# Kernel optimization log

Measured on AMD Instinct MI355X. Metric: run time of the kernel, lower is better.

## Reference

```python
import jax, jax.numpy as jnp
import numpy as np
import math

S, B, L, D = 4096, 2048, 256, 128  # substructure pool, batch, max substructs/drug, hidden


def setup_inputs() -> dict:
    key = jax.random.key(0)
    ks = jax.random.split(key, 6)
    sub_feat = jax.random.normal(ks[0], (S, D), dtype=jnp.float32)
    sub_index = jax.random.randint(ks[1], (B, L), 0, S)
    # ragged lengths -> padded prefix mask (1.0 = valid substructure)
    lengths = jax.random.randint(ks[2], (B,), 8, L + 1)
    mask = (jnp.arange(L)[None, :] < lengths[:, None]).astype(jnp.float32)
    scale = 1.0 / math.sqrt(D)
    Wq = jax.random.normal(ks[3], (D, D), dtype=jnp.float32) * scale
    Wk = jax.random.normal(ks[4], (D, D), dtype=jnp.float32) * scale
    bq = jnp.zeros((D,), dtype=jnp.float32)
    bk = jnp.zeros((D,), dtype=jnp.float32)
    return {"sub_feat": sub_feat, "mask": mask, "Wq": Wq, "bq": bq,
            "Wk": Wk, "bk": bk, "sub_index": sub_index}


def reference(sub_feat, mask, Wq, bq, Wk, bk, sub_index):
    # per-drug gather of substructure ('expert') features: [B, L, D]
    gathered = sub_feat[sub_index]
    # single-head Q/K projections (V is computed but unused in the original)
    q = gathered @ Wq + bq  # [B, L, D]
    k = gathered @ Wk + bk  # [B, L, D]
    inv_sqrt_d = 1.0 / math.sqrt(D)
    # additive mask: (1 - m) * -10000 broadcast over query dim
    add_mask = (1.0 - mask)[:, None, :] * -10000.0  # [B, 1, L]
    scores = jnp.einsum('bid,bjd->bij', q, k) * inv_sqrt_d + add_mask  # [B, L, L]
    probs = jax.nn.softmax(scores, axis=-1)
    # O[:, 0, 0, :] in the original: head 0, query position 0
    score = probs[:, 0, :]  # [B, L]
    # drug_feat[i] = score[i] @ sub_feat[sub_index[i]]
    drug_embeddings = jnp.einsum('bl,bld->bd', score, gathered)  # [B, D]
    return drug_embeddings
```

## Files before the change

kernel.cpp:

```cpp
#include <hip/hip_runtime.h>

#define DIM 128
#define LEN 256
#define INV_SQRT_D 0.08838834764831845f
#define LOG2E 1.4426950408889634f
#define SCALE_L2 (INV_SQRT_D * LOG2E)

#define WS_MT   0
#define WS_C    (DIM * DIM)
#define WS_W2   (DIM * DIM + DIM)
#define WS_BQBK (DIM * DIM + 2 * DIM)
#define WS_VBUF (DIM * DIM + 2 * DIM + 8)

__global__ __launch_bounds__(128) void precompute_kernel(
    const float* __restrict__ Wq, const float* __restrict__ bq,
    const float* __restrict__ Wk, const float* __restrict__ bk,
    float* __restrict__ ws)
{
    const int t = threadIdx.x;
    const int j = blockIdx.x;
    if (j < DIM) {
        __shared__ float wqj[DIM];
        wqj[t] = Wq[j * DIM + t];
        __syncthreads();
        const float4* row = reinterpret_cast<const float4*>(Wk + t * DIM);
        float acc = 0.f;
        #pragma unroll 8
        for (int i = 0; i < DIM / 4; ++i) {
            float4 u = row[i];
            acc = fmaf(u.x, wqj[4*i+0], acc);
            acc = fmaf(u.y, wqj[4*i+1], acc);
            acc = fmaf(u.z, wqj[4*i+2], acc);
            acc = fmaf(u.w, wqj[4*i+3], acc);
        }
        ws[WS_MT + j * DIM + t] = acc;
    } else {
        __shared__ float bqs[DIM], bks[DIM], red[DIM];
        bqs[t] = bq[t]; bks[t] = bk[t];
        __syncthreads();
        const float4* rk = reinterpret_cast<const float4*>(Wk + t * DIM);
        const float4* rq = reinterpret_cast<const float4*>(Wq + t * DIM);
        float accC = 0.f, accW = 0.f;
        #pragma unroll 8
        for (int i = 0; i < DIM / 4; ++i) {
            float4 a  = rk[i];
            float4 b2 = rq[i];
            accC = fmaf(a.x,  bqs[4*i+0], accC);
            accC = fmaf(a.y,  bqs[4*i+1], accC);
            accC = fmaf(a.z,  bqs[4*i+2], accC);
            accC = fmaf(a.w,  bqs[4*i+3], accC);
            accW = fmaf(b2.x, bks[4*i+0], accW);
            accW = fmaf(b2.y, bks[4*i+1], accW);
            accW = fmaf(b2.z, bks[4*i+2], accW);
            accW = fmaf(b2.w, bks[4*i+3], accW);
        }
        ws[WS_C  + t] = accC;
        ws[WS_W2 + t] = accW;
        red[t] = bqs[t] * bks[t];
        __syncthreads();
        if (t == 0) {
            float s = 0.f;
            for (int i = 0; i < DIM; ++i) s += red[i];
            ws[WS_BQBK] = s;
        }
    }
}

__global__ __launch_bounds__(256) void vcompute_kernel(
    const float* __restrict__ sub_feat, const int* __restrict__ sub_index,
    const float* __restrict__ ws, float* __restrict__ vout,
    float* __restrict__ qout, int B)
{
    const int t    = threadIdx.x;
    const int lane = t & 63;
    const int wv   = t >> 6;

    __shared__ float MtL[DIM * DIM];
    __shared__ float g0L[4][DIM];

    const float4* Msrc = reinterpret_cast<const float4*>(ws + WS_MT);
    float4* Mdst = reinterpret_cast<float4*>(MtL);
    #pragma unroll
    for (int i = 0; i < 16; ++i) Mdst[t + 256 * i] = Msrc[t + 256 * i];
    __syncthreads();

    const float* w2 = ws + WS_W2;
    const float* cc = ws + WS_C;
    const float  bqbk = ws[WS_BQBK];

    #pragma unroll
    for (int s = 0; s < 2; ++s) {
        const int b = blockIdx.x * 8 + wv * 2 + s;
        if (b >= B) break;
        const int r0 = sub_index[(size_t)b * LEN];
        const float2 g0p = reinterpret_cast<const float2*>(sub_feat + (size_t)r0 * DIM)[lane];
        g0L[wv][2 * lane]     = g0p.x;
        g0L[wv][2 * lane + 1] = g0p.y;

        float qp = g0p.x * w2[2 * lane] + g0p.y * w2[2 * lane + 1];
        #pragma unroll
        for (int o = 32; o > 0; o >>= 1) qp += __shfl_xor(qp, o);
        if (lane == 0) qout[b] = qp + bqbk;

        float a0 = 0.f, a1 = 0.f;
        #pragma unroll 8
        for (int j = 0; j < DIM; ++j) {
            const float g = g0L[wv][j];
            a0 = fmaf(g, MtL[j * DIM + lane],      a0);
            a1 = fmaf(g, MtL[j * DIM + lane + 64], a1);
        }
        vout[(size_t)b * DIM + lane]      = a0 + cc[lane];
        vout[(size_t)b * DIM + lane + 64] = a1 + cc[lane + 64];
    }
}

__global__ __launch_bounds__(256) void attn_kernel(
    const float* __restrict__ sub_feat, const float* __restrict__ mask,
    const int* __restrict__ sub_index, const float* __restrict__ vbuf,
    const float* __restrict__ qbuf, float* __restrict__ out, int B)
{
    const int t    = threadIdx.x;
    const int lane = t & 63;
    const int wv   = t >> 6;
    const int pair = wv >> 1;
    const int rhalf= wv & 1;
    const int b    = blockIdx.x * 2 + pair;
    const int g    = lane >> 4;
    const int m16  = lane & 15;

    __shared__ int   idxs[4][DIM];
    __shared__ float bias[4][DIM];
    __shared__ float OW  [4][DIM];
    __shared__ float Zw  [4];

    float Zr = 0.f;
    float O0=0.f,O1=0.f,O2=0.f,O3=0.f,O4=0.f,O5=0.f,O6=0.f,O7=0.f;

    if (b < B) {
        int*   idw = idxs[wv];
        float* bw  = bias[wv];
        const int*   ib = sub_index + (size_t)b * LEN + rhalf * DIM;
        const float* mb = mask      + (size_t)b * LEN + rhalf * DIM;
        idw[lane]      = ib[lane];
        idw[lane + 64] = ib[lane + 64];
        bw[lane]       = (1.f - mb[lane])      * (-10000.f * LOG2E);
        bw[lane + 64]  = (1.f - mb[lane + 64]) * (-10000.f * LOG2E);

        const float4 vA = reinterpret_cast<const float4*>(vbuf + (size_t)b * DIM)[m16];
        const float4 vB = reinterpret_cast<const float4*>(vbuf + (size_t)b * DIM)[m16 + 16];
        const float qterm = qbuf[b] * SCALE_L2;

        #pragma unroll 4
        for (int k = 0; k < 32; ++k) {
            const int jl = 4 * k + g;
            const int ij = idw[jl];
            const float bj = bw[jl];
            const float* rp = sub_feat + (size_t)ij * DIM + 4 * m16;
            const float4 u0 = *reinterpret_cast<const float4*>(rp);
            const float4 u1 = *reinterpret_cast<const float4*>(rp + 64);
            float sd = u0.x*vA.x + u0.y*vA.y + u0.z*vA.z + u0.w*vA.w
                     + u1.x*vB.x + u1.y*vB.y + u1.z*vB.z + u1.w*vB.w;
            sd += __shfl_xor(sd, 1);
            sd += __shfl_xor(sd, 2);
            sd += __shfl_xor(sd, 4);
            sd += __shfl_xor(sd, 8);
            const float e = exp2f(sd * SCALE_L2 + qterm + bj);
            Zr += e;
            O0 = fmaf(e, u0.x, O0); O1 = fmaf(e, u0.y, O1);
            O2 = fmaf(e, u0.z, O2); O3 = fmaf(e, u0.w, O3);
            O4 = fmaf(e, u1.x, O4); O5 = fmaf(e, u1.y, O5);
            O6 = fmaf(e, u1.z, O6); O7 = fmaf(e, u1.w, O7);
        }

        #pragma unroll
        for (int msk = 16; msk <= 32; msk <<= 1) {
            Zr += __shfl_xor(Zr, msk);
            O0 += __shfl_xor(O0, msk); O1 += __shfl_xor(O1, msk);
            O2 += __shfl_xor(O2, msk); O3 += __shfl_xor(O3, msk);
            O4 += __shfl_xor(O4, msk); O5 += __shfl_xor(O5, msk);
            O6 += __shfl_xor(O6, msk); O7 += __shfl_xor(O7, msk);
        }
        if (lane < 16) {
            reinterpret_cast<float4*>(&OW[wv][0])[m16]  = make_float4(O0, O1, O2, O3);
            reinterpret_cast<float4*>(&OW[wv][64])[m16] = make_float4(O4, O5, O6, O7);
        }
        if (lane == 0) Zw[wv] = Zr;
    }
    __syncthreads();

    {
        const int p = t >> 7;
        const int d = t & (DIM - 1);
        const int ob = blockIdx.x * 2 + p;
        if (ob < B) {
            const float Zt = Zw[2*p] + Zw[2*p+1];
            out[(size_t)ob * DIM + d] = (OW[2*p][d] + OW[2*p+1][d]) / Zt;
        }
    }
}

__global__ __launch_bounds__(256) void fused_fallback(
    const float* __restrict__ sub_feat, const float* __restrict__ mask,
    const int* __restrict__ sub_index, const float* __restrict__ ws,
    float* __restrict__ out)
{
    const int t    = threadIdx.x;
    const int lane = t & 63;
    const int wv   = t >> 6;
    const int pair = wv >> 1;
    const int rhalf= wv & 1;
    const int b    = blockIdx.x * 2 + pair;
    const int c32  = lane & 31;
    const int h    = lane >> 5;
    const int g    = lane >> 4;
    const int m16  = lane & 15;

    const float* Mt = ws + WS_MT;
    const float* cc = ws + WS_C;
    const float* w2 = ws + WS_W2;

    __shared__ float g0s [4][DIM];
    __shared__ int   idxs[4][DIM];
    __shared__ float bias[4][DIM];
    __shared__ float OW  [4][DIM];
    __shared__ float Zw  [4];

    float* g0w = g0s[wv];
    int*   idw = idxs[wv];
    float* bw  = bias[wv];

    const int*   ib = sub_index + (size_t)b * LEN + rhalf * DIM;
    const float* mb = mask      + (size_t)b * LEN + rhalf * DIM;
    idw[lane]      = ib[lane];
    idw[lane + 64] = ib[lane + 64];
    bw[lane]       = (1.f - mb[lane])      * (-10000.f * LOG2E);
    bw[lane + 64]  = (1.f - mb[lane + 64]) * (-10000.f * LOG2E);

    const int r0 = sub_index[(size_t)b * LEN];
    const float2 g0p = reinterpret_cast<const float2*>(sub_feat + (size_t)r0 * DIM)[lane];
    g0w[2 * lane]     = g0p.x;
    g0w[2 * lane + 1] = g0p.y;

    float qp = g0p.x * w2[2 * lane] + g0p.y * w2[2 * lane + 1];
    #pragma unroll
    for (int o = 32; o > 0; o >>= 1) qp += __shfl_xor(qp, o);
    const float qterm = (qp + ws[WS_BQBK]) * SCALE_L2;

    float4 vacc = make_float4(0.f, 0.f, 0.f, 0.f);
    {
        const int jb = h * 64;
        #pragma unroll 8
        for (int k = 0; k < 64; ++k) {
            const int j = jb + k;
            const float gg = g0w[j];
            const float4 u = reinterpret_cast<const float4*>(Mt + j * DIM)[c32];
            vacc.x = fmaf(gg, u.x, vacc.x);
            vacc.y = fmaf(gg, u.y, vacc.y);
            vacc.z = fmaf(gg, u.z, vacc.z);
            vacc.w = fmaf(gg, u.w, vacc.w);
        }
    }
    vacc.x += __shfl_xor(vacc.x, 32);
    vacc.y += __shfl_xor(vacc.y, 32);
    vacc.z += __shfl_xor(vacc.z, 32);
    vacc.w += __shfl_xor(vacc.w, 32);
    const float4 cv = reinterpret_cast<const float4*>(cc)[c32];
    float4 vt;
    vt.x = vacc.x + cv.x; vt.y = vacc.y + cv.y;
    vt.z = vacc.z + cv.z; vt.w = vacc.w + cv.w;

    float4 vA, vB;
    vA.x = __shfl(vt.x, m16);      vA.y = __shfl(vt.y, m16);
    vA.z = __shfl(vt.z, m16);      vA.w = __shfl(vt.w, m16);
    vB.x = __shfl(vt.x, m16 + 16); vB.y = __shfl(vt.y, m16 + 16);
    vB.z = __shfl(vt.z, m16 + 16); vB.w = __shfl(vt.w, m16 + 16);

    float Zr = 0.f;
    float O0=0.f,O1=0.f,O2=0.f,O3=0.f,O4=0.f,O5=0.f,O6=0.f,O7=0.f;
    #pragma unroll 4
    for (int k = 0; k < 32; ++k) {
        const int jl = 4 * k + g;
        const int ij = idw[jl];
        const float bj = bw[jl];
        const float* rp = sub_feat + (size_t)ij * DIM + 4 * m16;
        const float4 u0 = *reinterpret_cast<const float4*>(rp);
        const float4 u1 = *reinterpret_cast<const float4*>(rp + 64);
        float sd = u0.x*vA.x + u0.y*vA.y + u0.z*vA.z + u0.w*vA.w
                 + u1.x*vB.x + u1.y*vB.y + u1.z*vB.z + u1.w*vB.w;
        sd += __shfl_xor(sd, 1);
        sd += __shfl_xor(sd, 2);
        sd += __shfl_xor(sd, 4);
        sd += __shfl_xor(sd, 8);
        const float e = exp2f(sd * SCALE_L2 + qterm + bj);
        Zr += e;
        O0 = fmaf(e, u0.x, O0); O1 = fmaf(e, u0.y, O1);
        O2 = fmaf(e, u0.z, O2); O3 = fmaf(e, u0.w, O3);
        O4 = fmaf(e, u1.x, O4); O5 = fmaf(e, u1.y, O5);
        O6 = fmaf(e, u1.z, O6); O7 = fmaf(e, u1.w, O7);
    }
    #pragma unroll
    for (int msk = 16; msk <= 32; msk <<= 1) {
        Zr += __shfl_xor(Zr, msk);
        O0 += __shfl_xor(O0, msk); O1 += __shfl_xor(O1, msk);
        O2 += __shfl_xor(O2, msk); O3 += __shfl_xor(O3, msk);
        O4 += __shfl_xor(O4, msk); O5 += __shfl_xor(O5, msk);
        O6 += __shfl_xor(O6, msk); O7 += __shfl_xor(O7, msk);
    }
    if (lane < 16) {
        reinterpret_cast<float4*>(&OW[wv][0])[m16]  = make_float4(O0, O1, O2, O3);
        reinterpret_cast<float4*>(&OW[wv][64])[m16] = make_float4(O4, O5, O6, O7);
    }
    if (lane == 0) Zw[wv] = Zr;
    __syncthreads();

    {
        const int p = t >> 7;
        const int d = t & (DIM - 1);
        const float Zt = Zw[2*p] + Zw[2*p+1];
        out[((size_t)blockIdx.x * 2 + p) * DIM + d] = (OW[2*p][d] + OW[2*p+1][d]) / Zt;
    }
}

extern "C" void kernel_launch(void* const* d_in, const int* in_sizes, int n_in,
                              void* d_out, int out_size, void* d_ws, size_t ws_size,
                              hipStream_t stream) {
    const float* sub_feat  = (const float*)d_in[0];
    const float* mask      = (const float*)d_in[1];
    const float* Wq        = (const float*)d_in[2];
    const float* bq        = (const float*)d_in[3];
    const float* Wk        = (const float*)d_in[4];
    const float* bk        = (const float*)d_in[5];
    const int*   sub_index = (const int*)d_in[6];
    float* outp = (float*)d_out;
    float* ws   = (float*)d_ws;

    const int B = in_sizes[6] / LEN;
    const size_t needed = ((size_t)WS_VBUF + (size_t)B * DIM + (size_t)B) * sizeof(float);

    precompute_kernel<<<dim3(DIM + 1), dim3(DIM), 0, stream>>>(Wq, bq, Wk, bk, ws);

    if (ws_size >= needed) {
        float* vbuf = ws + WS_VBUF;
        float* qbuf = vbuf + (size_t)B * DIM;
        vcompute_kernel<<<dim3((B + 7) / 8), dim3(256), 0, stream>>>(
            sub_feat, sub_index, ws, vbuf, qbuf, B);
        attn_kernel<<<dim3((B + 1) / 2), dim3(256), 0, stream>>>(
            sub_feat, mask, sub_index, vbuf, qbuf, outp, B);
    } else {
        fused_fallback<<<dim3(B / 2), dim3(256), 0, stream>>>(
            sub_feat, mask, sub_index, ws, outp);
    }
}
```

Before: 32.47 us.

## Gather bf16 copy of substructure features in attention and fold scale into V/q

A new kernel converts sub_feat to bf16 each call. The attention kernel then gathers 16-byte rows of 8 bf16 values instead of two float4 loads, which halves gather traffic. The softmax scale is pre-multiplied into vbuf and qbuf, which removes a multiply from the inner loop. The attention kernel is also regrouped to one drug per 256-thread block, with four waves splitting the 256 positions, and sets occupancy launch bounds. The costs are an extra launch and reduced precision of the features used in the scores and the weighted sum.

```diff
diff --git a/kernel.cpp b/kernel.cpp
--- a/kernel.cpp
+++ b/kernel.cpp
@@ -11,6 +11,9 @@
 #define WS_W2   (DIM * DIM + DIM)
 #define WS_BQBK (DIM * DIM + 2 * DIM)
 #define WS_VBUF (DIM * DIM + 2 * DIM + 8)
+
+__device__ __forceinline__ float bl(unsigned u) { return __uint_as_float(u << 16); }
+__device__ __forceinline__ float bh(unsigned u) { return __uint_as_float(u & 0xffff0000u); }
 
 __global__ __launch_bounds__(128) void precompute_kernel(
     const float* __restrict__ Wq, const float* __restrict__ bq,
@@ -66,6 +69,22 @@
     }
 }
 
+__global__ __launch_bounds__(256) void convert_kernel(
+    const float* __restrict__ src, ushort* __restrict__ dst, int n4)
+{
+    const int i = blockIdx.x * 256 + threadIdx.x;
+    if (i < n4) {
+        const float4 u = reinterpret_cast<const float4*>(src)[i];
+        ushort4 o;
+        unsigned a;
+        a = __float_as_uint(u.x); o.x = (ushort)((a + 0x7fffu + ((a >> 16) & 1u)) >> 16);
+        a = __float_as_uint(u.y); o.y = (ushort)((a + 0x7fffu + ((a >> 16) & 1u)) >> 16);
+        a = __float_as_uint(u.z); o.z = (ushort)((a + 0x7fffu + ((a >> 16) & 1u)) >> 16);
+        a = __float_as_uint(u.w); o.w = (ushort)((a + 0x7fffu + ((a >> 16) & 1u)) >> 16);
+        reinterpret_cast<ushort4*>(dst)[i] = o;
+    }
+}
+
 __global__ __launch_bounds__(256) void vcompute_kernel(
     const float* __restrict__ sub_feat, const int* __restrict__ sub_index,
     const float* __restrict__ ws, float* __restrict__ vout,
@@ -100,7 +119,7 @@
         float qp = g0p.x * w2[2 * lane] + g0p.y * w2[2 * lane + 1];
         #pragma unroll
         for (int o = 32; o > 0; o >>= 1) qp += __shfl_xor(qp, o);
-        if (lane == 0) qout[b] = qp + bqbk;
+        if (lane == 0) qout[b] = (qp + bqbk) * SCALE_L2;
 
         float a0 = 0.f, a1 = 0.f;
         #pragma unroll 8
@@ -109,93 +128,80 @@
             a0 = fmaf(g, MtL[j * DIM + lane],      a0);
             a1 = fmaf(g, MtL[j * DIM + lane + 64], a1);
         }
-        vout[(size_t)b * DIM + lane]      = a0 + cc[lane];
-        vout[(size_t)b * DIM + lane + 64] = a1 + cc[lane + 64];
-    }
-}
-
-__global__ __launch_bounds__(256) void attn_kernel(
-    const float* __restrict__ sub_feat, const float* __restrict__ mask,
+        vout[(size_t)b * DIM + lane]      = (a0 + cc[lane])      * SCALE_L2;
+        vout[(size_t)b * DIM + lane + 64] = (a1 + cc[lane + 64]) * SCALE_L2;
+    }
+}
+
+__global__ __launch_bounds__(256, 8) void attn_kernel(
+    const ushort* __restrict__ gfeat, const float* __restrict__ mask,
     const int* __restrict__ sub_index, const float* __restrict__ vbuf,
-    const float* __restrict__ qbuf, float* __restrict__ out, int B)
+    const float* __restrict__ qbuf, float* __restrict__ out)
 {
     const int t    = threadIdx.x;
     const int lane = t & 63;
     const int wv   = t >> 6;
-    const int pair = wv >> 1;
-    const int rhalf= wv & 1;
-    const int b    = blockIdx.x * 2 + pair;
+    const int b    = blockIdx.x;
     const int g    = lane >> 4;
     const int m16  = lane & 15;
 
-    __shared__ int   idxs[4][DIM];
-    __shared__ float bias[4][DIM];
-    __shared__ float OW  [4][DIM];
-    __shared__ float Zw  [4];
+    __shared__ int   idw[LEN];
+    __shared__ float bw [LEN];
+    __shared__ float OW [4][DIM];
+    __shared__ float Zw [4];
+
+    idw[t] = sub_index[(size_t)b * LEN + t];
+    bw[t]  = (1.f - mask[(size_t)b * LEN + t]) * (-10000.f * LOG2E);
+
+    const float4 va = reinterpret_cast<const float4*>(vbuf + (size_t)b * DIM)[2 * m16];
+    const float4 vb = reinterpret_cast<const float4*>(vbuf + (size_t)b * DIM)[2 * m16 + 1];
+    const float qterm = qbuf[b];
 
     float Zr = 0.f;
     float O0=0.f,O1=0.f,O2=0.f,O3=0.f,O4=0.f,O5=0.f,O6=0.f,O7=0.f;
 
-    if (b < B) {
-        int*   idw = idxs[wv];
-        float* bw  = bias[wv];
-        const int*   ib = sub_index + (size_t)b * LEN + rhalf * DIM;
-        const float* mb = mask      + (size_t)b * LEN + rhalf * DIM;
-        idw[lane]      = ib[lane];
-        idw[lane + 64] = ib[lane + 64];
-        bw[lane]       = (1.f - mb[lane])      * (-10000.f * LOG2E);
-        bw[lane + 64]  = (1.f - mb[lane + 64]) * (-10000.f * LOG2E);
-
-        const float4 vA = reinterpret_cast<const float4*>(vbuf + (size_t)b * DIM)[m16];
-        const float4 vB = reinterpret_cast<const float4*>(vbuf + (size_t)b * DIM)[m16 + 16];
-        const float qterm = qbuf[b] * SCALE_L2;
-
-        #pragma unroll 4
-        for (int k = 0; k < 32; ++k) {
-            const int jl = 4 * k + g;
-            const int ij = idw[jl];
-            const float bj = bw[jl];
-            const float* rp = sub_feat + (size_t)ij * DIM + 4 * m16;
-            const float4 u0 = *reinterpret_cast<const float4*>(rp);
-            const float4 u1 = *reinterpret_cast<const float4*>(rp + 64);
-            float sd = u0.x*vA.x + u0.y*vA.y + u0.z*vA.z + u0.w*vA.w
-                     + u1.x*vB.x + u1.y*vB.y + u1.z*vB.z + u1.w*vB.w;
-            sd += __shfl_xor(sd, 1);
-            sd += __shfl_xor(sd, 2);
-            sd += __shfl_xor(sd, 4);
-            sd += __shfl_xor(sd, 8);
-            const float e = exp2f(sd * SCALE_L2 + qterm + bj);
-            Zr += e;
-            O0 = fmaf(e, u0.x, O0); O1 = fmaf(e, u0.y, O1);
-            O2 = fmaf(e, u0.z, O2); O3 = fmaf(e, u0.w, O3);
-            O4 = fmaf(e, u1.x, O4); O5 = fmaf(e, u1.y, O5);
-            O6 = fmaf(e, u1.z, O6); O7 = fmaf(e, u1.w, O7);
-        }
-
-        #pragma unroll
-        for (int msk = 16; msk <= 32; msk <<= 1) {
-            Zr += __shfl_xor(Zr, msk);
-            O0 += __shfl_xor(O0, msk); O1 += __shfl_xor(O1, msk);
-            O2 += __shfl_xor(O2, msk); O3 += __shfl_xor(O3, msk);
-            O4 += __shfl_xor(O4, msk); O5 += __shfl_xor(O5, msk);
-            O6 += __shfl_xor(O6, msk); O7 += __shfl_xor(O7, msk);
-        }
-        if (lane < 16) {
-            reinterpret_cast<float4*>(&OW[wv][0])[m16]  = make_float4(O0, O1, O2, O3);
-            reinterpret_cast<float4*>(&OW[wv][64])[m16] = make_float4(O4, O5, O6, O7);
-        }
-        if (lane == 0) Zw[wv] = Zr;
-    }
+    const int jbase = wv * 64;
+    #pragma unroll 4
+    for (int k = 0; k < 16; ++k) {
+        const int jl = jbase + 4 * k + g;
+        const int ij = idw[jl];
+        const float bj = bw[jl];
+        const uint4 u = *reinterpret_cast<const uint4*>(gfeat + (size_t)ij * DIM + 8 * m16);
+        const float f0 = bl(u.x), f1 = bh(u.x), f2 = bl(u.y), f3 = bh(u.y);
+        const float f4 = bl(u.z), f5 = bh(u.z), f6 = bl(u.w), f7 = bh(u.w);
+        float sd = f0*va.x + f1*va.y + f2*va.z + f3*va.w
+                 + f4*vb.x + f5*vb.y + f6*vb.z + f7*vb.w;
+        sd += __shfl_xor(sd, 1);
+        sd += __shfl_xor(sd, 2);
+        sd += __shfl_xor(sd, 4);
+        sd += __shfl_xor(sd, 8);
+        const float e = exp2f(sd + qterm + bj);
+        Zr += e;
+        O0 = fmaf(e, f0, O0); O1 = fmaf(e, f1, O1);
+        O2 = fmaf(e, f2, O2); O3 = fmaf(e, f3, O3);
+        O4 = fmaf(e, f4, O4); O5 = fmaf(e, f5, O5);
+        O6 = fmaf(e, f6, O6); O7 = fmaf(e, f7, O7);
+    }
+
+    #pragma unroll
+    for (int msk = 16; msk <= 32; msk <<= 1) {
+        Zr += __shfl_xor(Zr, msk);
+        O0 += __shfl_xor(O0, msk); O1 += __shfl_xor(O1, msk);
+        O2 += __shfl_xor(O2, msk); O3 += __shfl_xor(O3, msk);
+        O4 += __shfl_xor(O4, msk); O5 += __shfl_xor(O5, msk);
+        O6 += __shfl_xor(O6, msk); O7 += __shfl_xor(O7, msk);
+    }
+    if (lane < 16) {
+        reinterpret_cast<float4*>(&OW[wv][0])[2 * m16]     = make_float4(O0, O1, O2, O3);
+        reinterpret_cast<float4*>(&OW[wv][0])[2 * m16 + 1] = make_float4(O4, O5, O6, O7);
+    }
+    if (lane == 0) Zw[wv] = Zr;
     __syncthreads();
 
-    {
-        const int p = t >> 7;
-        const int d = t & (DIM - 1);
-        const int ob = blockIdx.x * 2 + p;
-        if (ob < B) {
-            const float Zt = Zw[2*p] + Zw[2*p+1];
-            out[(size_t)ob * DIM + d] = (OW[2*p][d] + OW[2*p+1][d]) / Zt;
-        }
+    if (t < DIM) {
+        const float Zt = Zw[0] + Zw[1] + Zw[2] + Zw[3];
+        out[(size_t)b * DIM + t] =
+            (OW[0][t] + OW[1][t] + OW[2][t] + OW[3][t]) / Zt;
     }
 }
 
@@ -227,14 +233,14 @@
 
     float* g0w = g0s[wv];
     int*   idw = idxs[wv];
-    float* bw  = bias[wv];
+    float* bww = bias[wv];
 
     const int*   ib = sub_index + (size_t)b * LEN + rhalf * DIM;
     const float* mb = mask      + (size_t)b * LEN + rhalf * DIM;
     idw[lane]      = ib[lane];
     idw[lane + 64] = ib[lane + 64];
-    bw[lane]       = (1.f - mb[lane])      * (-10000.f * LOG2E);
-    bw[lane + 64]  = (1.f - mb[lane + 64]) * (-10000.f * LOG2E);
+    bww[lane]      = (1.f - mb[lane])      * (-10000.f * LOG2E);
+    bww[lane + 64] = (1.f - mb[lane + 64]) * (-10000.f * LOG2E);
 
     const int r0 = sub_index[(size_t)b * LEN];
     const float2 g0p = reinterpret_cast<const float2*>(sub_feat + (size_t)r0 * DIM)[lane];
@@ -266,8 +272,8 @@
     vacc.w += __shfl_xor(vacc.w, 32);
     const float4 cv = reinterpret_cast<const float4*>(cc)[c32];
     float4 vt;
-    vt.x = vacc.x + cv.x; vt.y = vacc.y + cv.y;
-    vt.z = vacc.z + cv.z; vt.w = vacc.w + cv.w;
+    vt.x = (vacc.x + cv.x) * SCALE_L2; vt.y = (vacc.y + cv.y) * SCALE_L2;
+    vt.z = (vacc.z + cv.z) * SCALE_L2; vt.w = (vacc.w + cv.w) * SCALE_L2;
 
     float4 vA, vB;
     vA.x = __shfl(vt.x, m16);      vA.y = __shfl(vt.y, m16);
@@ -281,7 +287,7 @@
     for (int k = 0; k < 32; ++k) {
         const int jl = 4 * k + g;
         const int ij = idw[jl];
-        const float bj = bw[jl];
+        const float bj = bww[jl];
         const float* rp = sub_feat + (size_t)ij * DIM + 4 * m16;
         const float4 u0 = *reinterpret_cast<const float4*>(rp);
         const float4 u1 = *reinterpret_cast<const float4*>(rp + 64);
@@ -291,7 +297,7 @@
         sd += __shfl_xor(sd, 2);
         sd += __shfl_xor(sd, 4);
         sd += __shfl_xor(sd, 8);
-        const float e = exp2f(sd * SCALE_L2 + qterm + bj);
+        const float e = exp2f(sd + qterm + bj);
         Zr += e;
         O0 = fmaf(e, u0.x, O0); O1 = fmaf(e, u0.y, O1);
         O2 = fmaf(e, u0.z, O2); O3 = fmaf(e, u0.w, O3);
@@ -334,18 +340,25 @@
     float* outp = (float*)d_out;
     float* ws   = (float*)d_ws;
 
-    const int B = in_sizes[6] / LEN;
-    const size_t needed = ((size_t)WS_VBUF + (size_t)B * DIM + (size_t)B) * sizeof(float);
+    const int B  = in_sizes[6] / LEN;
+    const int SD = in_sizes[0];
+
+    const size_t WS_BF = (size_t)WS_VBUF + (size_t)B * DIM + (size_t)B;
+    const size_t needed = (WS_BF + (size_t)(SD + 1) / 2) * sizeof(float);
 
     precompute_kernel<<<dim3(DIM + 1), dim3(DIM), 0, stream>>>(Wq, bq, Wk, bk, ws);
 
     if (ws_size >= needed) {
-        float* vbuf = ws + WS_VBUF;
-        float* qbuf = vbuf + (size_t)B * DIM;
+        float*  vbuf = ws + WS_VBUF;
+        float*  qbuf = vbuf + (size_t)B * DIM;
+        ushort* bfb  = reinterpret_cast<ushort*>(ws + WS_BF);
+
+        convert_kernel<<<dim3((SD / 4 + 255) / 256), dim3(256), 0, stream>>>(
+            sub_feat, bfb, SD / 4);
         vcompute_kernel<<<dim3((B + 7) / 8), dim3(256), 0, stream>>>(
             sub_feat, sub_index, ws, vbuf, qbuf, B);
-        attn_kernel<<<dim3((B + 1) / 2), dim3(256), 0, stream>>>(
-            sub_feat, mask, sub_index, vbuf, qbuf, outp, B);
+        attn_kernel<<<dim3(B), dim3(256), 0, stream>>>(
+            bfb, mask, sub_index, vbuf, qbuf, outp);
     } else {
         fused_fallback<<<dim3(B / 2), dim3(256), 0, stream>>>(
             sub_feat, mask, sub_index, ws, outp);
```

Measured after the change: 34.95 us. 7.7% more time.
